# Optimization experiments

Measured on AMD Instinct MI355X. Metric: run time of the kernel, lower is better.

## Reference

```python
import jax, jax.numpy as jnp
import numpy as np

SCALE = 4
FEAT = 64
BANDS = 10
HID = 256
HEADS = 4
K = 7
K2 = K * K
GATE_TAU = 1.0
B, HL, WL = 1, 80, 80
IN_DIM = FEAT + 4 * BANDS + 2  # 106


def conv2d(x, w, b, groups=1):
    y = jax.lax.conv_general_dilated(
        x, w, window_strides=(1, 1), padding='SAME',
        dimension_numbers=('NCHW', 'OIHW', 'NCHW'), feature_group_count=groups)
    return y + b[None, :, None, None]


def _gray(t):
    return 0.2989 * t[:, 0:1] + 0.587 * t[:, 1:2] + 0.114 * t[:, 2:3]


def setup_inputs() -> dict:
    key = jax.random.key(0)
    ks = jax.random.split(key, 12)
    rn = lambda k, shape, s: jax.random.normal(k, shape, dtype=jnp.float32) * s
    return {
        'lr': jax.random.uniform(ks[0], (B, 3, HL, WL), dtype=jnp.float32),
        'enc_w0': rn(ks[1], (FEAT, 3, 3, 3), 0.1), 'enc_b0': jnp.zeros((FEAT,), jnp.float32),
        'enc_wh': rn(ks[2], (3, FEAT, FEAT, 3, 3), 0.05), 'enc_bh': jnp.zeros((3, FEAT), jnp.float32),
        'mlp_w0': rn(ks[3], (IN_DIM, HID), 0.05), 'mlp_b0': jnp.zeros((HID,), jnp.float32),
        'mlp_wh': rn(ks[4], (4, HID, HID), 0.05), 'mlp_bh': jnp.zeros((4, HID), jnp.float32),
        'kern_w': rn(ks[5], (HID, HEADS * K2), 0.05), 'kern_b': jnp.zeros((HEADS * K2,), jnp.float32),
        'gate_w': rn(ks[6], (HID, HEADS), 0.05), 'gate_b': jnp.zeros((HEADS,), jnp.float32),
        'ref_w0': rn(ks[7], (48, 2, 3, 3), 0.1), 'ref_b0': jnp.zeros((48,), jnp.float32),
        'ref_w1': rn(ks[8], (48, 16, 3, 3), 0.05), 'ref_b1': jnp.zeros((48,), jnp.float32),
        'ref_w2': rn(ks[9], (3, 16, 3, 3), 0.05), 'ref_b2': jnp.zeros((3,), jnp.float32),
    }


def reference(lr, enc_w0, enc_b0, enc_wh, enc_bh, mlp_w0, mlp_b0, mlp_wh, mlp_bh,
              kern_w, kern_b, gate_w, gate_b, ref_w0, ref_b0, ref_w1, ref_b1, ref_w2, ref_b2):
    Bn, _, hl, wl = lr.shape
    HH, WH = hl * SCALE, wl * SCALE
    f = jax.nn.gelu(conv2d(lr, enc_w0, enc_b0))
    for i in range(enc_wh.shape[0]):
        f = jax.nn.gelu(conv2d(f, enc_wh[i], enc_bh[i]))
    # ---- bicubic upsample to HR ----
    lr_up = jax.image.resize(lr, (Bn, 3, HH, WH), method='cubic')
    # ---- HR integer grid -> normalized coords, LR continuous coords ----
    ys, xs = jnp.meshgrid(jnp.arange(HH, dtype=jnp.float32), jnp.arange(WH, dtype=jnp.float32), indexing='ij')
    hx = xs.reshape(-1); hy = ys.reshape(-1)  # [N]
    hxn = (hx + 0.5) / WH * 2.0 - 1.0
    hyn = (hy + 0.5) / HH * 2.0 - 1.0
    lx = (hx + 0.5) / SCALE - 0.5
    ly = (hy + 0.5) / SCALE - 0.5
    bx = jnp.floor(lx); by = jnp.floor(ly)
    fx = lx - bx; fy = ly - by  # frac in [0,1)
    bxi = jnp.clip(bx, 0, wl - 1).astype(jnp.int32)
    byi = jnp.clip(by, 0, hl - 1).astype(jnp.int32)
    # ---- Fourier PE: per band [sin x, cos x, sin y, cos y] ----
    freqs = (2.0 ** jnp.arange(BANDS, dtype=jnp.float32)) * jnp.pi
    px = hxn[:, None] * freqs
    py = hyn[:, None] * freqs
    pe = jnp.stack([jnp.sin(px), jnp.cos(px), jnp.sin(py), jnp.cos(py)], axis=2).reshape(-1, 4 * BANDS)
    N = pe.shape[0]
    # ---- gather center LR features ----
    idx_c = byi * wl + bxi  # [N]
    cfeat = jnp.take(f.reshape(Bn, FEAT, hl * wl), idx_c, axis=2).transpose(0, 2, 1)  # [B,N,C]
    frac = jnp.stack([fx, fy], axis=1)  # [N,2]
    x = jnp.concatenate([cfeat,
                         jnp.broadcast_to(pe[None], (Bn, N, 4 * BANDS)),
                         jnp.broadcast_to(frac[None], (Bn, N, 2))], axis=-1)
    # ---- KernelMLP ----
    h = jax.nn.gelu(x @ mlp_w0 + mlp_b0)
    for i in range(mlp_wh.shape[0]):
        h = jax.nn.gelu(h @ mlp_wh[i] + mlp_bh[i])
    kwts = jax.nn.softmax((h @ kern_w + kern_b).reshape(Bn, N, HEADS, K2), axis=-1)
    gate = jax.nn.softmax((h @ gate_w + gate_b) / GATE_TAU, axis=-1)  # [B,N,H]
    # ---- KxK RGB neighborhood gather (clamped borders) ----
    r = K // 2
    oy, ox = jnp.meshgrid(jnp.arange(-r, r + 1), jnp.arange(-r, r + 1), indexing='ij')
    ox = ox.reshape(-1); oy = oy.reshape(-1)  # [K2]
    nx = jnp.clip(bxi[:, None] + ox[None, :], 0, wl - 1)
    ny = jnp.clip(byi[:, None] + oy[None, :], 0, hl - 1)
    idx_n = (ny * wl + nx).reshape(-1)  # [N*K2]
    neigh = jnp.take(lr.reshape(Bn, 3, hl * wl), idx_n, axis=2).reshape(Bn, 3, N, K2)
    # ---- dynamic weighted sum: kernels per head, gated head mixture ----
    res0 = jnp.einsum('bcnk,bnhk,bnh->bcn', neigh, kwts, gate).reshape(Bn, 3, HH, WH)
    # ---- color-safe residual refiner (groups=3) ----
    ref_in = jnp.concatenate([lr_up, res0], axis=1)
    hr = jax.nn.gelu(conv2d(ref_in, ref_w0, ref_b0, groups=3))
    hr = jax.nn.gelu(conv2d(hr, ref_w1, ref_b1, groups=3))
    res_ref = conv2d(hr, ref_w2, ref_b2, groups=3)
    sr = jnp.clip(lr_up + res0 + res_ref, 0.0, 1.0)
    # ---- color-preserving fusion ----
    delta = _gray(sr) - _gray(lr_up)
    return jnp.clip(lr_up + jnp.broadcast_to(delta, (Bn, 3, HH, WH)), 0.0, 1.0)
```

## Files before the change

kernel.cpp:

```cpp
#include <hip/hip_runtime.h>
#include <math.h>


#define HL 80
#define WL 80
#define HH 320
#define WH 320
#define NPIX (HH*WH)
#define LRPIX (HL*WL)
#define HID 256
#define K2 49

typedef _Float16 half8 __attribute__((ext_vector_type(8)));
typedef _Float16 half4 __attribute__((ext_vector_type(4)));
typedef float f32x4 __attribute__((ext_vector_type(4)));

__device__ __forceinline__ float gelu_f(float x) {
  float u = __builtin_fmaf(0.044715f*x, x*x, x);
  float e = __expf(-1.5957691216057308f * u);
  return x * __builtin_amdgcn_rcpf(1.0f + e);
}

__device__ __forceinline__ float keys_cubic(float x) {
  x = fabsf(x);
  if (x >= 2.0f) return 0.0f;
  if (x >= 1.0f) return ((-0.5f*x + 2.5f)*x - 4.0f)*x + 2.0f;
  return ((1.5f*x - 2.5f)*x)*x + 1.0f;
}

__global__ void enc_conv0(const float* __restrict__ in, const float* __restrict__ w,
                          const float* __restrict__ bias, float* __restrict__ out) {
  __shared__ float wl[216];
  int tid = threadIdx.x;
  int chunk = blockIdx.y;
  if (tid < 216) {
    int o = tid/27, r = tid - o*27, ic = r/9, tap = r - ic*9;
    wl[tap*24 + ic*8 + o] = w[((chunk*8+o)*3+ic)*9 + tap];
  }
  __syncthreads();
  int pix = blockIdx.x*blockDim.x + tid;
  int y = pix / WL, x = pix % WL;
  float acc[8];
#pragma unroll
  for (int o=0;o<8;o++) acc[o] = bias[chunk*8+o];
#pragma unroll
  for (int ky=0; ky<3; ky++) {
    int yy = y+ky-1;
    if (yy < 0 || yy >= HL) continue;
#pragma unroll
    for (int kx=0; kx<3; kx++) {
      int xx = x+kx-1;
      if (xx < 0 || xx >= WL) continue;
      int o0 = yy*WL+xx, tap = ky*3+kx;
#pragma unroll
      for (int ic=0; ic<3; ic++) {
        float v = in[ic*LRPIX + o0];
        const f32x4* wb = (const f32x4*)&wl[tap*24 + ic*8];
        f32x4 w0 = wb[0], w1 = wb[1];
#pragma unroll
        for (int o=0;o<4;o++) { acc[o] += v*w0[o]; acc[o+4] += v*w1[o]; }
      }
    }
  }
#pragma unroll
  for (int o=0;o<8;o++)
    out[pix*64 + chunk*8 + o] = gelu_f(acc[o]);
}

__global__ void enc_convh(const float* __restrict__ in, const float* __restrict__ w,
                          const float* __restrict__ bias, float* __restrict__ out) {
  __shared__ float wl[4608];
  int tid = threadIdx.x;
  int chunk = blockIdx.y;
  const float* wsrc = w + chunk*8*576;
#pragma unroll
  for (int i=0;i<36;i++) {
    int idx = tid + i*128;
    int o = idx/576, r = idx - o*576, ic = r/9, tap = r - ic*9;
    wl[tap*512 + ic*8 + o] = wsrc[idx];
  }
  __syncthreads();
  int pix = blockIdx.x*128 + tid;
  int y = pix / WL, x = pix % WL;
  float acc[8];
#pragma unroll
  for (int o=0;o<8;o++) acc[o] = bias[chunk*8+o];
#pragma unroll
  for (int ky=0; ky<3; ky++) {
    int yy = y+ky-1;
    if (yy < 0 || yy >= HL) continue;
#pragma unroll
    for (int kx=0; kx<3; kx++) {
      int xx = x+kx-1;
      if (xx < 0 || xx >= WL) continue;
      const f32x4* src = (const f32x4*)&in[(yy*WL+xx)*64];
      const float* wt = &wl[(ky*3+kx)*512];
#pragma unroll
      for (int icv=0; icv<16; icv++) {
        f32x4 v = src[icv];
#pragma unroll
        for (int j=0;j<4;j++) {
          const f32x4* wb = (const f32x4*)&wt[(icv*4+j)*8];
          f32x4 w0 = wb[0], w1 = wb[1];
#pragma unroll
          for (int o=0;o<4;o++) { acc[o] += v[j]*w0[o]; acc[4+o] += v[j]*w1[o]; }
        }
      }
    }
  }
#pragma unroll
  for (int o=0;o<8;o++)
    out[pix*64 + chunk*8 + o] = gelu_f(acc[o]);
}

__global__ void bicubic_up(const float* __restrict__ lr, float* __restrict__ up) {
  int id = blockIdx.x*blockDim.x + threadIdx.x;
  if (id >= 3*NPIX) return;
  int c = id / NPIX, p = id % NPIX;
  int hy = p / WH, hx = p % WH;
  float sx = (hx+0.5f)*0.25f - 0.5f;
  float sy = (hy+0.5f)*0.25f - 0.5f;
  int bx = (int)floorf(sx), by = (int)floorf(sy);
  float wx[4], wy[4];
  int ix[4], iy[4];
  float sumx = 0.f, sumy = 0.f;
#pragma unroll
  for (int i=0;i<4;i++) {
    int j = bx-1+i;
    float wv = (j>=0 && j<WL) ? keys_cubic(sx - (float)j) : 0.f;
    wx[i] = wv; ix[i] = min(max(j,0), WL-1); sumx += wv;
    j = by-1+i;
    wv = (j>=0 && j<HL) ? keys_cubic(sy - (float)j) : 0.f;
    wy[i] = wv; iy[i] = min(max(j,0), HL-1); sumy += wv;
  }
  float inx = __builtin_amdgcn_rcpf(sumx), iny = __builtin_amdgcn_rcpf(sumy);
  const float* src = lr + c*LRPIX;
  float acc = 0.f;
#pragma unroll
  for (int i=0;i<4;i++) {
    float rowv = 0.f;
#pragma unroll
    for (int j=0;j<4;j++) rowv += wx[j]*src[iy[i]*WL + ix[j]];
    acc += wy[i]*rowv;
  }
  up[c*NPIX + p] = acc * inx * iny;
}

__global__ void prep_weights(const float* __restrict__ w0, const float* __restrict__ wh,
                             const float* __restrict__ kw, const float* __restrict__ gw,
                             _Float16* __restrict__ out) {
  int idx = blockIdx.x*blockDim.x + threadIdx.x;
  int e = idx & 7, lane = (idx>>3)&63;
  int kf = (lane>>4)*8 + e;
  int nf = lane & 15;
  if (idx < 32768) {
    int t = idx >> 9;
    int kt = t & 3, nt = t >> 2;
    int k = kt*32 + kf, n = nt*16 + nf;
    out[idx] = (_Float16)((k < 106) ? w0[k*HID + n] : 0.f);
  } else if (idx < 32768 + 4*65536) {
    int r = idx - 32768;
    int L = r >> 16; r &= 65535;
    int t = r >> 9;
    int kt = t & 7, nt = t >> 3;
    int k = kt*32 + kf, n = nt*16 + nf;
    out[idx] = (_Float16)wh[(L*HID + k)*HID + n];
  } else if (idx < 32768 + 5*65536) {
    int r = idx - (32768 + 4*65536);
    int t = r >> 9;
    int kt = t & 7, nt = t >> 3;
    int k = kt*32 + kf, n = nt*16 + nf;
    float v = (n < 196) ? kw[k*196 + n] : ((n < 200) ? gw[k*4 + (n-196)] : 0.f);
    out[idx] = (_Float16)v;
  }
}

#define PMT 512
__global__ __launch_bounds__(PMT, 4)
void pixel_mlp2(const float* __restrict__ f, const float* __restrict__ lr,
                const _Float16* __restrict__ Wt0, const float* __restrict__ b0,
                const _Float16* __restrict__ Wth, const float* __restrict__ bh,
                const _Float16* __restrict__ Whd, const float* __restrict__ kb,
                const float* __restrict__ gb, float* __restrict__ res0) {
  __shared__ _Float16 smem[8192 + 16384 + 16384];
  _Float16* x_lds = smem;
  _Float16* hA    = smem + 8192;
  _Float16* hB    = smem + 8192 + 16384;
  _Float16* kbuf  = hB;

  const int tid = threadIdx.x;
  const int lane = tid & 63;
  const int wave = tid >> 6;
  const int n0 = blockIdx.x * 64;
  const int hy = n0 / WH;
  const int hx0 = n0 % WH;
  const float ly = (hy+0.5f)*0.25f - 0.5f;
  const int byi = min(max((int)floorf(ly),0), HL-1);
  const float fy = ly - floorf(ly);
  const float hyn = (hy+0.5f)/320.0f*2.0f - 1.0f;

#pragma unroll
  for (int i = 0; i < 8; i++) {
    int p = (tid>>6) + i*8;
    int k = lane;
    int hx = hx0 + p;
    float lx = (hx+0.5f)*0.25f - 0.5f;
    int bxi = min(max((int)floorf(lx),0), WL-1);
    float v = f[(byi*WL + bxi)*64 + k];
    x_lds[p*128 + (k ^ ((p&7)<<3))] = (_Float16)v;
  }
#pragma unroll
  for (int i = 0; i < 8; i++) {
    int p = (tid>>6) + i*8;
    int k = 64 + lane;
    int hx = hx0 + p;
    float v = 0.f;
    if (k < 104) {
      int band = (k-64) >> 2, r = (k-64) & 3;
      float freq = (float)(1<<band) * 3.14159265358979323846f;
      float hxn = (hx+0.5f)/320.0f*2.0f - 1.0f;
      float arg = ((r<2) ? hxn : hyn) * freq;
      v = (r&1) ? cosf(arg) : sinf(arg);
    } else if (k == 104) {
      float lx = (hx+0.5f)*0.25f - 0.5f;
      v = lx - floorf(lx);
    } else if (k == 105) {
      v = fy;
    }
    x_lds[p*128 + (k ^ ((p&7)<<3))] = (_Float16)v;
  }
  __syncthreads();

  const int col  = lane & 15;
  const int koff = (lane>>4)*8;
  const int sw   = (lane&7)<<3;
  const int rbase = (lane>>4)*4;

  f32x4 acc[2][4];
  const f32x4 vzero = {0.f,0.f,0.f,0.f};
  const half8* A0 = (const half8*)Wt0;
  const half8* AH = (const half8*)Whd;

#pragma unroll
  for (int nt=0;nt<2;nt++)
#pragma unroll
    for (int pt=0;pt<4;pt++) acc[nt][pt] = vzero;
#pragma unroll
  for (int ks=0; ks<4; ks++) {
    int k0 = ks*32 + koff;
    half8 aw[2], bx[4];
#pragma unroll
    for (int nt=0;nt<2;nt++)
      aw[nt] = A0[((wave*2+nt)*4 + ks)*64 + lane];
#pragma unroll
    for (int pt=0;pt<4;pt++)
      bx[pt] = *(const half8*)&x_lds[(pt*16+col)*128 + (k0 ^ sw)];
#pragma unroll
    for (int nt=0;nt<2;nt++)
#pragma unroll
      for (int pt=0;pt<4;pt++)
        acc[nt][pt] = __builtin_amdgcn_mfma_f32_16x16x32_f16(aw[nt], bx[pt], acc[nt][pt], 0,0,0);
  }
#pragma unroll
  for (int nt=0;nt<2;nt++) {
    int nbase = wave*32 + nt*16 + rbase;
    f32x4 bb = *(const f32x4*)&b0[nbase];
#pragma unroll
    for (int pt=0;pt<4;pt++) {
      int pix = pt*16 + col;
      half4 hv;
      hv[0] = (_Float16)gelu_f(acc[nt][pt][0] + bb[0]);
      hv[1] = (_Float16)gelu_f(acc[nt][pt][1] + bb[1]);
      hv[2] = (_Float16)gelu_f(acc[nt][pt][2] + bb[2]);
      hv[3] = (_Float16)gelu_f(acc[nt][pt][3] + bb[3]);
      *(half4*)&hA[pix*256 + (nbase ^ sw)] = hv;
    }
  }
  __syncthreads();

  for (int L=0; L<4; L++) {
    const _Float16* hs = (L & 1) ? hB : hA;
    _Float16*       hd = (L & 1) ? hA : hB;
    const half8* AL = (const half8*)(Wth + L*65536);
#pragma unroll
    for (int nt=0;nt<2;nt++)
#pragma unroll
      for (int pt=0;pt<4;pt++) acc[nt][pt] = vzero;
#pragma unroll
    for (int ks=0; ks<8; ks++) {
      int k0 = ks*32 + koff;
      half8 aw[2], bx[4];
#pragma unroll
      for (int nt=0;nt<2;nt++)
        aw[nt] = AL[((wave*2+nt)*8 + ks)*64 + lane];
#pragma unroll
      for (int pt=0;pt<4;pt++)
        bx[pt] = *(const half8*)&hs[(pt*16+col)*256 + (k0 ^ sw)];
#pragma unroll
      for (int nt=0;nt<2;nt++)
#pragma unroll
        for (int pt=0;pt<4;pt++)
          acc[nt][pt] = __builtin_amdgcn_mfma_f32_16x16x32_f16(aw[nt], bx[pt], acc[nt][pt], 0,0,0);
    }
#pragma unroll
    for (int nt=0;nt<2;nt++) {
      int nbase = wave*32 + nt*16 + rbase;
      f32x4 bb = *(const f32x4*)&bh[L*HID + nbase];
#pragma unroll
      for (int pt=0;pt<4;pt++) {
        int pix = pt*16 + col;
        half4 hv;
        hv[0] = (_Float16)gelu_f(acc[nt][pt][0] + bb[0]);
        hv[1] = (_Float16)gelu_f(acc[nt][pt][1] + bb[1]);
        hv[2] = (_Float16)gelu_f(acc[nt][pt][2] + bb[2]);
        hv[3] = (_Float16)gelu_f(acc[nt][pt][3] + bb[3]);
        *(half4*)&hd[pix*256 + (nbase ^ sw)] = hv;
      }
    }
    __syncthreads();
  }

#pragma unroll
  for (int nt=0;nt<2;nt++)
#pragma unroll
    for (int pt=0;pt<4;pt++) acc[nt][pt] = vzero;
#pragma unroll
  for (int ks=0; ks<8; ks++) {
    int k0 = ks*32 + koff;
    half8 aw[2], bx[4];
#pragma unroll
    for (int nt=0;nt<2;nt++)
      aw[nt] = AH[((wave*2+nt)*8 + ks)*64 + lane];
#pragma unroll
    for (int pt=0;pt<4;pt++)
      bx[pt] = *(const half8*)&hA[(pt*16+col)*256 + (k0 ^ sw)];
#pragma unroll
    for (int nt=0;nt<2;nt++)
#pragma unroll
      for (int pt=0;pt<4;pt++)
        acc[nt][pt] = __builtin_amdgcn_mfma_f32_16x16x32_f16(aw[nt], bx[pt], acc[nt][pt], 0,0,0);
  }
#pragma unroll
  for (int nt=0;nt<2;nt++) {
    int jb = wave*32 + nt*16 + rbase;
    if (jb < 200) {
      const float* bp = (jb < 196) ? (kb + jb) : (gb + (jb - 196));
      f32x4 bb = *(const f32x4*)bp;
#pragma unroll
      for (int pt=0;pt<4;pt++) {
        int pix = pt*16 + col;
        half4 kv;
        kv[0] = (_Float16)(acc[nt][pt][0] + bb[0]);
        kv[1] = (_Float16)(acc[nt][pt][1] + bb[1]);
        kv[2] = (_Float16)(acc[nt][pt][2] + bb[2]);
        kv[3] = (_Float16)(acc[nt][pt][3] + bb[3]);
        *(half4*)&kbuf[pix*208 + jb] = kv;
      }
    }
  }
  __syncthreads();

  {
    int p = tid >> 3, q = tid & 7;
    int h = q & 3, part = q >> 2;
    int hx = hx0 + p;
    float lx = (hx+0.5f)*0.25f - 0.5f;
    int bxi = min(max((int)floorf(lx),0), WL-1);
    const _Float16* kp = &kbuf[p*208];
    float g0=(float)kp[196], g1=(float)kp[197], g2=(float)kp[198], g3=(float)kp[199];
    float gm = fmaxf(fmaxf(g0,g1), fmaxf(g2,g3));
    g0=__expf(g0-gm); g1=__expf(g1-gm); g2=__expf(g2-gm); g3=__expf(g3-gm);
    float gs = __builtin_amdgcn_rcpf(g0+g1+g2+g3);
    float gate[4] = {g0*gs, g1*gs, g2*gs, g3*gs};
    const int t0 = part*25;
    const int cnt = part ? 24 : 25;
    float rv[25];
#pragma unroll
    for (int i=0;i<25;i++) rv[i] = (i<cnt) ? (float)kp[h*K2 + t0 + i] : -1e30f;
    float mh = rv[0];
#pragma unroll
    for (int i=1;i<25;i++) mh = fmaxf(mh, rv[i]);
    mh = fmaxf(mh, __shfl_xor(mh, 4));
    float sh = 0.f;
#pragma unroll
    for (int i=0;i<25;i++)
      if (i<cnt) sh += __expf(rv[i]-mh);
    sh += __shfl_xor(sh, 4);
    int base = lane & ~7;
    float m[4], gos[4];
#pragma unroll
    for (int hh=0; hh<4; hh++) {
      m[hh]  = __shfl(mh, base+hh);
      float sv = __shfl(sh, base+hh);
      gos[hh] = gate[hh]*__builtin_amdgcn_rcpf(sv);
    }
    float r0=0.f, r1=0.f, r2=0.f;
    if (q < 7) {
      int dy = q-3;
      int ny = min(max(byi+dy,0),HL-1);
#pragma unroll
      for (int i=0;i<7;i++) {
        int t = q*7+i;
        int nx = min(max(bxi+i-3,0),WL-1);
        float wq = gos[0]*__expf((float)kp[t]-m[0]) + gos[1]*__expf((float)kp[K2+t]-m[1])
                 + gos[2]*__expf((float)kp[2*K2+t]-m[2]) + gos[3]*__expf((float)kp[3*K2+t]-m[3]);
        int o = ny*WL + nx;
        r0 += wq*lr[o]; r1 += wq*lr[LRPIX+o]; r2 += wq*lr[2*LRPIX+o];
      }
    }
#pragma unroll
    for (int msk=1; msk<8; msk<<=1) {
      r0 += __shfl_xor(r0, msk);
      r1 += __shfl_xor(r1, msk);
      r2 += __shfl_xor(r2, msk);
    }
    if (q == 0) {
      int n = n0 + p;
      res0[n] = r0; res0[NPIX+n] = r1; res0[2*NPIX+n] = r2;
    }
  }
}

__global__ void rconv0(const float* __restrict__ lrup, const float* __restrict__ res0,
                       const float* __restrict__ w, const float* __restrict__ bias,
                       float* __restrict__ out) {
  __shared__ float wl[288];
  int tid = threadIdx.x;
  int g = blockIdx.y;
  for (int idx = tid; idx < 288; idx += 256) {
    int o = idx/18, r = idx - o*18, ic = r/9, tap = r - ic*9;
    wl[tap*32 + ic*16 + o] = w[((g*16+o)*2+ic)*9 + tap];
  }
  __syncthreads();
  int p = blockIdx.x*blockDim.x + tid;
  int y = p / WH, x = p % WH;
  float acc[16];
#pragma unroll
  for (int o=0;o<16;o++) acc[o] = bias[g*16+o];
#pragma unroll
  for (int ky=0;ky<3;ky++) {
    int yy = y+ky-1;
    if (yy<0||yy>=HH) continue;
#pragma unroll
    for (int kx=0;kx<3;kx++) {
      int xx = x+kx-1;
      if (xx<0||xx>=WH) continue;
      int o0 = yy*WH+xx, tap = ky*3+kx;
#pragma unroll
      for (int ic=0; ic<2; ic++) {
        float v = (ic==0 ? lrup : res0)[g*NPIX + o0];
        const f32x4* wb = (const f32x4*)&wl[tap*32 + ic*16];
#pragma unroll
        for (int ov=0; ov<4; ov++) {
          f32x4 wv = wb[ov];
#pragma unroll
          for (int oo=0; oo<4; oo++) acc[ov*4+oo] += v*wv[oo];
        }
      }
    }
  }
  float* dst = out + p*48 + g*16;
#pragma unroll
  for (int o=0;o<16;o++) dst[o] = gelu_f(acc[o]);
}

__global__ void rconv1(const float* __restrict__ hr0, const float* __restrict__ w,
                       const float* __restrict__ bias, float* __restrict__ out) {
  __shared__ float wl[2304];
  int tid = threadIdx.x;
  int g = blockIdx.y;
  const float* wsrc = w + g*2304;
#pragma unroll
  for (int i=0;i<9;i++) {
    int idx = tid + i*256;
    int o = idx/144, r = idx - o*144, ic = r/9, tap = r - ic*9;
    wl[tap*256 + ic*16 + o] = wsrc[idx];
  }
  __syncthreads();
  int p = blockIdx.x*blockDim.x + tid;
  int y = p / WH, x = p % WH;
  float acc[16];
#pragma unroll
  for (int o=0;o<16;o++) acc[o] = bias[g*16+o];
#pragma unroll
  for (int ky=0;ky<3;ky++) {
    int yy = y+ky-1;
    if (yy<0||yy>=HH) continue;
#pragma unroll
    for (int kx=0;kx<3;kx++) {
      int xx = x+kx-1;
      if (xx<0||xx>=WH) continue;
      const f32x4* src = (const f32x4*)&hr0[(yy*WH+xx)*48 + g*16];
      const float* wt = &wl[(ky*3+kx)*256];
#pragma unroll
      for (int icv=0; icv<4; icv++) {
        f32x4 v = src[icv];
#pragma unroll
        for (int j=0;j<4;j++) {
          const f32x4* wb = (const f32x4*)&wt[(icv*4+j)*16];
#pragma unroll
          for (int ov=0; ov<4; ov++) {
            f32x4 wv = wb[ov];
#pragma unroll
            for (int oo=0; oo<4; oo++) acc[ov*4+oo] += v[j]*wv[oo];
          }
        }
      }
    }
  }
  float* dst = out + p*48 + g*16;
#pragma unroll
  for (int o=0;o<16;o++) dst[o] = gelu_f(acc[o]);
}

__global__ void rconv2_fuse(const float* __restrict__ hr1, const float* __restrict__ lrup,
                            const float* __restrict__ res0, const float* __restrict__ w,
                            const float* __restrict__ bias, float* __restrict__ out) {
  __shared__ float wl[432];
  int tid = threadIdx.x;
  for (int idx = tid; idx < 432; idx += 256) {
    int c = idx/144, r = idx - c*144, ic = r/9, tap = r - ic*9;
    wl[tap*48 + c*16 + ic] = w[idx];
  }
  __syncthreads();
  int p = blockIdx.x*blockDim.x + tid;
  if (p >= NPIX) return;
  int y = p / WH, x = p % WH;
  float acc3[3];
#pragma unroll
  for (int c=0;c<3;c++) acc3[c] = bias[c];
#pragma unroll
  for (int ky=0;ky<3;ky++) {
    int yy=y+ky-1; if (yy<0||yy>=HH) continue;
#pragma unroll
    for (int kx=0;kx<3;kx++) {
      int xx=x+kx-1; if (xx<0||xx>=WH) continue;
      const f32x4* src = (const f32x4*)&hr1[(yy*WH+xx)*48];
      const float* wt = &wl[(ky*3+kx)*48];
#pragma unroll
      for (int c=0;c<3;c++) {
#pragma unroll
        for (int icv=0; icv<4; icv++) {
          f32x4 v = src[c*4 + icv];
          f32x4 wv = *(const f32x4*)&wt[c*16 + icv*4];
          acc3[c] += v[0]*wv[0] + v[1]*wv[1] + v[2]*wv[2] + v[3]*wv[3];
        }
      }
    }
  }
  float sr[3], lu[3];
#pragma unroll
  for (int c=0;c<3;c++) {
    float l = lrup[c*NPIX+p];
    lu[c]=l;
    float srv = l + res0[c*NPIX+p] + acc3[c];
    sr[c] = fminf(fmaxf(srv,0.f),1.f);
  }
  float delta = 0.2989f*(sr[0]-lu[0]) + 0.587f*(sr[1]-lu[1]) + 0.114f*(sr[2]-lu[2]);
#pragma unroll
  for (int c=0;c<3;c++)
    out[c*NPIX+p] = fminf(fmaxf(lu[c]+delta,0.f),1.f);
}

extern "C" void kernel_launch(void* const* d_in, const int* in_sizes, int n_in,
                              void* d_out, int out_size, void* d_ws, size_t ws_size,
                              hipStream_t stream) {
  const float* lr     = (const float*)d_in[0];
  const float* enc_w0 = (const float*)d_in[1];
  const float* enc_b0 = (const float*)d_in[2];
  const float* enc_wh = (const float*)d_in[3];
  const float* enc_bh = (const float*)d_in[4];
  const float* mlp_w0 = (const float*)d_in[5];
  const float* mlp_b0 = (const float*)d_in[6];
  const float* mlp_wh = (const float*)d_in[7];
  const float* mlp_bh = (const float*)d_in[8];
  const float* kern_w = (const float*)d_in[9];
  const float* kern_b = (const float*)d_in[10];
  const float* gate_w = (const float*)d_in[11];
  const float* gate_b = (const float*)d_in[12];
  const float* ref_w0 = (const float*)d_in[13];
  const float* ref_b0 = (const float*)d_in[14];
  const float* ref_w1 = (const float*)d_in[15];
  const float* ref_b1 = (const float*)d_in[16];
  const float* ref_w2 = (const float*)d_in[17];
  const float* ref_b2 = (const float*)d_in[18];
  float* out = (float*)d_out;
  float* ws = (float*)d_ws;

  float* f_a  = ws;
  float* f_b  = ws + 409600;
  float* lrup = ws + 819200;
  float* res0 = ws + 1126400;
  float* hr0  = ws + 1433600;
  float* hr1  = ws + 6348800;

  _Float16* Wt0 = (_Float16*)f_a;
  _Float16* Wth = Wt0 + 32768;
  _Float16* Whd = Wth + 4*65536;

  enc_conv0<<<dim3(25,8), 256, 0, stream>>>(lr, enc_w0, enc_b0, f_a);
  enc_convh<<<dim3(50,8), 128, 0, stream>>>(f_a, enc_wh + 0*36864, enc_bh + 0,   f_b);
  enc_convh<<<dim3(50,8), 128, 0, stream>>>(f_b, enc_wh + 1*36864, enc_bh + 64,  f_a);
  enc_convh<<<dim3(50,8), 128, 0, stream>>>(f_a, enc_wh + 2*36864, enc_bh + 128, f_b);

  bicubic_up<<<1200, 256, 0, stream>>>(lr, lrup);

  prep_weights<<<1408, 256, 0, stream>>>(mlp_w0, mlp_wh, kern_w, gate_w, Wt0);

  pixel_mlp2<<<1600, PMT, 0, stream>>>(f_b, lr, Wt0, mlp_b0, Wth, mlp_bh,
                                       Whd, kern_b, gate_b, res0);

  rconv0<<<dim3(400,3), 256, 0, stream>>>(lrup, res0, ref_w0, ref_b0, hr0);
  rconv1<<<dim3(400,3), 256, 0, stream>>>(hr0, ref_w1, ref_b1, hr1);
  rconv2_fuse<<<400, 256, 0, stream>>>(hr1, lrup, res0, ref_w2, ref_b2, out);
}
```

Measured before the change: 307.4 us.

## Compute neighborhood softmax per row lane and split refiner activations by group

The dynamic-kernel softmax is restructured. Each of the 7 row lanes now loads its own 7 taps for all 4 heads, computes max and sum with xor shuffles across the 8 lanes, and reuses the stored exponentials in the weighted sum. Before, the work was split by head and half and every tap's exponential was computed a second time. Separately, the refiner's intermediate activations change from pixel-interleaved [pixel][48] to group-planar [group][pixel][16], so each group's conv reads a contiguous 64-byte run per pixel. The softmax change trades more registers for fewer exp calls and loads.

```diff
diff --git a/kernel.cpp b/kernel.cpp
--- a/kernel.cpp
+++ b/kernel.cpp
@@ -362,7 +362,6 @@
 
   {
     int p = tid >> 3, q = tid & 7;
-    int h = q & 3, part = q >> 2;
     int hx = hx0 + p;
     float lx = (hx+0.5f)*0.25f - 0.5f;
     int bxi = min(max((int)floorf(lx),0), WL-1);
@@ -372,38 +371,53 @@
     g0=__expf(g0-gm); g1=__expf(g1-gm); g2=__expf(g2-gm); g3=__expf(g3-gm);
     float gs = __builtin_amdgcn_rcpf(g0+g1+g2+g3);
     float gate[4] = {g0*gs, g1*gs, g2*gs, g3*gs};
-    const int t0 = part*25;
-    const int cnt = part ? 24 : 25;
-    float rv[25];
-#pragma unroll
-    for (int i=0;i<25;i++) rv[i] = (i<cnt) ? (float)kp[h*K2 + t0 + i] : -1e30f;
-    float mh = rv[0];
-#pragma unroll
-    for (int i=1;i<25;i++) mh = fmaxf(mh, rv[i]);
-    mh = fmaxf(mh, __shfl_xor(mh, 4));
-    float sh = 0.f;
-#pragma unroll
-    for (int i=0;i<25;i++)
-      if (i<cnt) sh += __expf(rv[i]-mh);
-    sh += __shfl_xor(sh, 4);
-    int base = lane & ~7;
-    float m[4], gos[4];
-#pragma unroll
-    for (int hh=0; hh<4; hh++) {
-      m[hh]  = __shfl(mh, base+hh);
-      float sv = __shfl(sh, base+hh);
-      gos[hh] = gate[hh]*__builtin_amdgcn_rcpf(sv);
-    }
+    float e[4][7];
+    float m[4];
+#pragma unroll
+    for (int h=0;h<4;h++) m[h] = -1e30f;
+    if (q < 7) {
+#pragma unroll
+      for (int h=0;h<4;h++)
+#pragma unroll
+        for (int i=0;i<7;i++) {
+          float v = (float)kp[h*K2 + q*7 + i];
+          e[h][i] = v;
+          m[h] = fmaxf(m[h], v);
+        }
+    }
+#pragma unroll
+    for (int h=0;h<4;h++) {
+      m[h] = fmaxf(m[h], __shfl_xor(m[h], 1));
+      m[h] = fmaxf(m[h], __shfl_xor(m[h], 2));
+      m[h] = fmaxf(m[h], __shfl_xor(m[h], 4));
+    }
+    float s[4] = {0.f,0.f,0.f,0.f};
+    if (q < 7) {
+#pragma unroll
+      for (int h=0;h<4;h++)
+#pragma unroll
+        for (int i=0;i<7;i++) {
+          float ev = __expf(e[h][i] - m[h]);
+          e[h][i] = ev;
+          s[h] += ev;
+        }
+    }
+#pragma unroll
+    for (int h=0;h<4;h++) {
+      s[h] += __shfl_xor(s[h], 1);
+      s[h] += __shfl_xor(s[h], 2);
+      s[h] += __shfl_xor(s[h], 4);
+    }
+    float gos[4];
+#pragma unroll
+    for (int h=0;h<4;h++) gos[h] = gate[h]*__builtin_amdgcn_rcpf(s[h]);
     float r0=0.f, r1=0.f, r2=0.f;
     if (q < 7) {
-      int dy = q-3;
-      int ny = min(max(byi+dy,0),HL-1);
+      int ny = min(max(byi + q - 3,0),HL-1);
 #pragma unroll
       for (int i=0;i<7;i++) {
-        int t = q*7+i;
         int nx = min(max(bxi+i-3,0),WL-1);
-        float wq = gos[0]*__expf((float)kp[t]-m[0]) + gos[1]*__expf((float)kp[K2+t]-m[1])
-                 + gos[2]*__expf((float)kp[2*K2+t]-m[2]) + gos[3]*__expf((float)kp[3*K2+t]-m[3]);
+        float wq = gos[0]*e[0][i] + gos[1]*e[1][i] + gos[2]*e[2][i] + gos[3]*e[3][i];
         int o = ny*WL + nx;
         r0 += wq*lr[o]; r1 += wq*lr[LRPIX+o]; r2 += wq*lr[2*LRPIX+o];
       }
@@ -459,7 +473,7 @@
       }
     }
   }
-  float* dst = out + p*48 + g*16;
+  float* dst = out + (g*NPIX + p)*16;
 #pragma unroll
   for (int o=0;o<16;o++) dst[o] = gelu_f(acc[o]);
 }
@@ -479,6 +493,7 @@
   __syncthreads();
   int p = blockIdx.x*blockDim.x + tid;
   int y = p / WH, x = p % WH;
+  const float* src_base = hr0 + g*NPIX*16;
   float acc[16];
 #pragma unroll
   for (int o=0;o<16;o++) acc[o] = bias[g*16+o];
@@ -490,7 +505,7 @@
     for (int kx=0;kx<3;kx++) {
       int xx = x+kx-1;
       if (xx<0||xx>=WH) continue;
-      const f32x4* src = (const f32x4*)&hr0[(yy*WH+xx)*48 + g*16];
+      const f32x4* src = (const f32x4*)&src_base[(yy*WH+xx)*16];
       const float* wt = &wl[(ky*3+kx)*256];
 #pragma unroll
       for (int icv=0; icv<4; icv++) {
@@ -508,7 +523,7 @@
       }
     }
   }
-  float* dst = out + p*48 + g*16;
+  float* dst = out + (g*NPIX + p)*16;
 #pragma unroll
   for (int o=0;o<16;o++) dst[o] = gelu_f(acc[o]);
 }
@@ -535,13 +550,14 @@
 #pragma unroll
     for (int kx=0;kx<3;kx++) {
       int xx=x+kx-1; if (xx<0||xx>=WH) continue;
-      const f32x4* src = (const f32x4*)&hr1[(yy*WH+xx)*48];
+      int o0 = yy*WH+xx;
       const float* wt = &wl[(ky*3+kx)*48];
 #pragma unroll
       for (int c=0;c<3;c++) {
+        const f32x4* src = (const f32x4*)&hr1[(c*NPIX + o0)*16];
 #pragma unroll
         for (int icv=0; icv<4; icv++) {
-          f32x4 v = src[c*4 + icv];
+          f32x4 v = src[icv];
           f32x4 wv = *(const f32x4*)&wt[c*16 + icv*4];
           acc3[c] += v[0]*wv[0] + v[1]*wv[1] + v[2]*wv[2] + v[3]*wv[3];
         }
```

Result: faster. 282.7 us (-8.0%).
